# Kernel optimization log

Measured on AMD Instinct MI355X. Metric: run time of the kernel, lower is better.

## Reference

```python
import jax, jax.numpy as jnp
import numpy as np
from jax import lax

# bior3.5 decomposition low-pass filter (pywt.Wavelet('bior3.5').dec_lo)
_BIOR35_DEC_LO = [-0.013810679320049757, 0.04143203796014927, 0.052480581416189075,
                  -0.26792717880896527, -0.07181553246425873, 0.966747552403483,
                  0.966747552403483, -0.07181553246425873, -0.26792717880896527,
                  0.052480581416189075, 0.04143203796014927, -0.013810679320049757]

J = 3  # decomposition levels


def setup_inputs() -> dict:
    key = jax.random.key(0)
    x = jax.random.normal(key, (16, 64, 16384), dtype=jnp.float32)
    hac = jnp.asarray(np.array(_BIOR35_DEC_LO, dtype=np.float32))
    return {"x": x, "hac": hac}


def _afb1d(x, h0, h1):
    """Analysis filter bank: stride-2 depthwise conv over last dim.

    x: (B, C, N); h0, h1: (L,). Returns (lo, hi), each (B, C, outsize).
    Since every channel uses the same pair of filters, we fold (B, C) into
    the batch dim and run a single-input-channel, 2-output-channel conv.
    """
    B, C, N = x.shape
    L = h0.shape[0]
    outsize = (N + L - 1) // 2              # pywt 'zero' mode coeff length
    p = 2 * (outsize - 1) - N + L           # total padding needed
    if p % 2 == 1:                          # odd -> extra zero on the right
        x = jnp.pad(x, ((0, 0), (0, 0), (0, 1)))
        N += 1
        p -= 1
    half = p // 2
    xr = x.reshape(B * C, 1, N)
    k = jnp.stack([h0, h1])[:, None, :]     # (2, 1, L) -- cross-correlation, like torch
    out = lax.conv_general_dilated(xr, k, window_strides=(2,),
                                   padding=[(half, half)],
                                   dimension_numbers=('NCH', 'OIH', 'NCH'))
    lo = out[:, 0, :].reshape(B, C, outsize)
    hi = out[:, 1, :].reshape(B, C, outsize)
    return lo, hi


def reference(x, hac):
    L = hac.shape[0]
    # QMF pair: h1[i] = (-1)^(i+1) * h0[L-1-i]  (miu[::2] = -1 in torch code)
    sign = jnp.where(jnp.arange(L) % 2 == 0, -1.0, 1.0).astype(hac.dtype)
    h0 = hac
    h1 = hac[::-1] * sign
    x0 = x
    highs = []
    for _ in range(J):
        x0, x1 = _afb1d(x0, h0, h1)
        highs.append(x1)
    return (x0, *highs)
```

## Files before the change

### kernel.cpp

```cpp
#include <hip/hip_runtime.h>


#define FILT_LEN 12
#define ROWS  1024
#define N1    16384
#define O1    8197
#define O2    4104
#define O3    2057
#define NBLK  8
#define T1    1025
#define T2    513
#define T3    258
#define NTHR  256

#define XCAP    2208
#define L1CAP   1120
#define LO2_OFF 1088
#define LO2SZ   560
#define HB2_OFF 1664
#define HI3_OFF 272

typedef float vf4 __attribute__((ext_vector_type(4)));
typedef float vf2 __attribute__((ext_vector_type(2)));

constexpr int cmin(int a, int b) { return a < b ? a : b; }
constexpr int cmax(int a, int b) { return a > b ? a : b; }

__device__ __forceinline__ int sw4(int f4) { return f4 ^ ((f4 >> 3) & 7); }
__device__ __forceinline__ float4 ld4(const float* p, int f4) {
    return reinterpret_cast<const float4*>(p)[sw4(f4)];
}
__device__ __forceinline__ void st4(float* p, int f4, float4 v) {
    reinterpret_cast<float4*>(p)[sw4(f4)] = v;
}
__device__ __forceinline__ float ldss(const float* p, int j) {
    return p[(sw4(j >> 2) << 2) | (j & 3)];
}
__device__ __forceinline__ void stss(float* p, int j, float v) {
    p[(sw4(j >> 2) << 2) | (j & 3)] = v;
}
__device__ __forceinline__ void stp2(float* p, int j, float a, float b) {
    *reinterpret_cast<float2*>(p + ((sw4(j >> 2) << 2) | (j & 3))) =
        make_float2(a, b);
}

__device__ __forceinline__ void bar_lgkm() {
    asm volatile("s_waitcnt lgkmcnt(0)" ::: "memory");
    __builtin_amdgcn_s_barrier();
    asm volatile("" ::: "memory");
}

__device__ __forceinline__ void ntst(float* p, float v) {
    __builtin_nontemporal_store(v, p);
}
__device__ __forceinline__ void ntst2(float* p, float a, float b) {
    vf2 v; v.x = a; v.y = b;
    __builtin_nontemporal_store(v, reinterpret_cast<vf2*>(p));
}
__device__ __forceinline__ void ntst4(float* p, float4 u) {
    vf4 v; v.x = u.x; v.y = u.y; v.z = u.z; v.w = u.w;
    __builtin_nontemporal_store(v, reinterpret_cast<vf4*>(p));
}

template<int LO, int HI, int SOFF>
__device__ __forceinline__ void flushv(const float* s, float* g, const int tid) {
    static_assert((SOFF & 3) == 0, "stash offset f4-aligned");
    constexpr int A  = (LO + 3) & ~3;
    constexpr int Bq = HI & ~3;
    if (tid < A - LO)
        ntst(g + LO + tid, ldss(s, SOFF + LO + tid));
    if (tid >= 4 && tid < 4 + (HI - Bq))
        ntst(g + Bq + (tid - 4), ldss(s, SOFF + Bq + (tid - 4)));
    for (int i = A + 4 * tid; i < Bq; i += 4 * NTHR)
        ntst4(g + i, ld4(s, (SOFF + i) >> 2));
}

template<int HI, int SOFF>
__device__ __forceinline__ void flush2(const float* s, float* g, const int tid) {
    static_assert((SOFF & 3) == 0, "stash offset f4-aligned");
    constexpr int Bq = HI & ~1;
    for (int i = 2 * tid; i < Bq; i += 2 * NTHR) {
        const float* q = s + ((sw4((SOFF + i) >> 2) << 2) | ((SOFF + i) & 3));
        ntst2(g + i, q[0], q[1]);
    }
    if ((HI & 1) && tid == 0) ntst(g + Bq, ldss(s, SOFF + Bq));
}

__device__ __forceinline__ constexpr float h0tap(int i) {
    constexpr float H[FILT_LEN] = {
        -0.013810679320049757f, 0.04143203796014927f, 0.052480581416189075f,
        -0.26792717880896527f, -0.07181553246425873f, 0.966747552403483f,
        0.966747552403483f, -0.07181553246425873f, -0.26792717880896527f,
        0.052480581416189075f, 0.04143203796014927f, -0.013810679320049757f};
    return H[i];
}
__device__ __forceinline__ constexpr float h1tap(int i) {
    return h0tap(FILT_LEN - 1 - i) * ((i & 1) ? 1.0f : -1.0f);
}
__device__ __forceinline__ vf2 tap2(int l) {
    vf2 t; t.x = h0tap(l); t.y = h1tap(l); return t;
}

__device__ __forceinline__ void pkfma(vf2& acc, float v, int l) {
#if __has_builtin(__builtin_elementwise_fma)
    vf2 vv; vv.x = v; vv.y = v;
    acc = __builtin_elementwise_fma(vv, tap2(l), acc);
#else
    acc.x = fmaf(v, h0tap(l), acc.x);
    acc.y = fmaf(v, h1tap(l), acc.y);
#endif
}

template<int B>
struct Cfg {
    static constexpr int s1 = B * T1, e1 = cmin(s1 + T1, O1);
    static constexpr int s2 = B * T2, e2 = cmin(s2 + T2, O2);
    static constexpr int s3 = B * T3, e3 = cmin(s3 + T3, O3);
    static constexpr int c2s = cmax(0, cmin(s2, 2 * s3 - 10)) & ~3;
    static constexpr int c2e = cmin(O2, cmax(e2, 2 * e3));
    static constexpr int c1s = cmax(0, cmin(s1, 2 * c2s - 10)) & ~3;
    static constexpr int c1e = cmin(O1, cmax(e1, 2 * c2e));
    static constexpr int span1 = c1e - c1s;
    static constexpr int span2 = c2e - c2s;
    static constexpr int span3 = e3 - s3;
    static constexpr int xbase = 2 * c1s - 12;
    static constexpr int D2 = 2 * c2s - 10 - c1s + 12;
    static constexpr int ab2 = D2 & ~3, p2 = D2 & 3;
    static constexpr int D3 = 2 * s3 - 10 - c2s + 12;
    static constexpr int ab3 = D3 & ~3, p3 = D3 & 3;
    static constexpr int zt1 = L1CAP - (12 + span1);
    static constexpr int zt2 = LO2SZ - (12 + span2);
    static constexpr int o1s = s1 - c1s, o1e = e1 - c1s;
    static constexpr int o2s = s2 - c2s, o2e = e2 - c2s;

    static_assert(D2 >= 0 && D3 >= 0, "pad origin");
    static_assert((D2 & 1) == 0 && (D3 & 1) == 0, "window parity (R5 bug)");
    static_assert(p2 <= 2 && p3 <= 2, "window shift fits window array");
    static_assert((c1s & 3) == 0 && (c2s & 3) == 0, "span starts mult-of-4");
    static_assert((xbase & 3) == 0, "x staging alignment");
    static_assert(zt1 >= 0 && zt1 <= NTHR, "l1 tail zero in one pass");
    static_assert(zt2 >= 0 && zt2 <= NTHR, "lo2 tail zero in one pass");
    static_assert(span1 <= 8 * NTHR, "L1 single K=8 pass");
    static_assert(span2 <= 4 * NTHR, "L2 single K=4 pass");
    static_assert(span3 <= 2 * NTHR, "L3 single K=2 pass");
    static_assert((span2 & 3) == 0, "L2 has no tail (store path)");
    static_assert(2 * (((span1 - 1) / 8) * 8) + 28 <= XCAP, "L1 window read");
    static_assert(2 * (((span2 - 1) / 4) * 4) + ab2 + 20 <= L1CAP, "L2 window read");
    static_assert(2 * (((span3 - 1) / 2) * 2) + ab3 + 16 <= LO2SZ, "L3 window read");
    static_assert(span1 <= LO2_OFF, "hi1 stash fits");
    static_assert(HB2_OFF + span2 <= XCAP, "hi2 stash fits");
    static_assert(HI3_OFF + span3 <= L1CAP, "hi3 stash fits");
    static_assert(HI3_OFF >= span3, "lo3/hi3 disjoint");
    static_assert(o1e <= span1 && o2e <= span2, "owned range inside span");
};

template<int B>
__device__ __forceinline__ void body(
    const float* __restrict__ xrow,
    float* __restrict__ lo3r, float* __restrict__ hi1r,
    float* __restrict__ hi2r, float* __restrict__ hi3r,
    float* __restrict__ xs, float* __restrict__ l1, const int tid)
{
    using C = Cfg<B>;

    if constexpr (C::xbase >= 0 && C::xbase + XCAP <= N1) {
        st4(xs, tid,       *reinterpret_cast<const float4*>(xrow + C::xbase + 4 * tid));
        st4(xs, tid + 256, *reinterpret_cast<const float4*>(xrow + C::xbase + 1024 + 4 * tid));
        if (tid < XCAP / 4 - 512)
            st4(xs, tid + 512, *reinterpret_cast<const float4*>(xrow + C::xbase + 2048 + 4 * tid));
    } else {
        for (int i = tid; i < XCAP / 4; i += NTHR) {
            const int g0 = C::xbase + 4 * i;
            float4 v;
            if (g0 >= 0 && g0 + 4 <= N1) {
                v = *reinterpret_cast<const float4*>(xrow + g0);
            } else {
                v.x = ((unsigned)(g0 + 0) < (unsigned)N1) ? xrow[g0 + 0] : 0.f;
                v.y = ((unsigned)(g0 + 1) < (unsigned)N1) ? xrow[g0 + 1] : 0.f;
                v.z = ((unsigned)(g0 + 2) < (unsigned)N1) ? xrow[g0 + 2] : 0.f;
                v.w = ((unsigned)(g0 + 3) < (unsigned)N1) ? xrow[g0 + 3] : 0.f;
            }
            st4(xs, i, v);
        }
    }
    if (tid < 12)      stss(l1, tid, 0.f);
    if (tid < C::zt1)  stss(l1, 12 + C::span1 + tid, 0.f);
    bar_lgkm();

    float hr1[8];
    const int tt1 = tid * 8;
    if (tt1 < C::span1) {
        float w[28];
#pragma unroll
        for (int m = 0; m < 7; ++m) {
            const float4 v = ld4(xs, tid * 4 + m);
            w[4 * m + 0] = v.x; w[4 * m + 1] = v.y;
            w[4 * m + 2] = v.z; w[4 * m + 3] = v.w;
        }
        vf2 ac[8];
#pragma unroll
        for (int k = 0; k < 8; ++k) { ac[k].x = 0.f; ac[k].y = 0.f; }
#pragma unroll
        for (int l = 0; l < FILT_LEN; ++l) {
#pragma unroll
            for (int k = 0; k < 8; ++k)
                pkfma(ac[k], w[2 * k + 2 + l], l);
        }
#pragma unroll
        for (int k = 0; k < 8; ++k) hr1[k] = ac[k].y;
        if (tt1 + 8 <= C::span1) {
            st4(l1, 3 + 2 * tid, make_float4(ac[0].x, ac[1].x, ac[2].x, ac[3].x));
            st4(l1, 4 + 2 * tid, make_float4(ac[4].x, ac[5].x, ac[6].x, ac[7].x));
        } else {
#pragma unroll
            for (int k = 0; k < 8; ++k)
                if (tt1 + k < C::span1) stss(l1, 12 + tt1 + k, ac[k].x);
        }
    }
    bar_lgkm();

    if (tt1 < C::span1) {
        if (tt1 + 8 <= C::span1) {
            st4(xs, 2 * tid,     make_float4(hr1[0], hr1[1], hr1[2], hr1[3]));
            st4(xs, 2 * tid + 1, make_float4(hr1[4], hr1[5], hr1[6], hr1[7]));
        } else {
#pragma unroll
            for (int k = 0; k < 8; ++k)
                if (tt1 + k < C::span1) stss(xs, tt1 + k, hr1[k]);
        }
    }
    if (tid < 12)      stss(xs, LO2_OFF + tid, 0.f);
    if (tid < C::zt2)  stss(xs, LO2_OFF + 12 + C::span2 + tid, 0.f);

    {
        const int tt2 = tid * 4;
        if (tt2 < C::span2) {
            float w[20];
#pragma unroll
            for (int m = 0; m < 5; ++m) {
                const float4 v = ld4(l1, tid * 2 + (C::ab2 >> 2) + m);
                w[4 * m + 0] = v.x; w[4 * m + 1] = v.y;
                w[4 * m + 2] = v.z; w[4 * m + 3] = v.w;
            }
            vf2 ac[4];
#pragma unroll
            for (int k = 0; k < 4; ++k) { ac[k].x = 0.f; ac[k].y = 0.f; }
#pragma unroll
            for (int l = 0; l < FILT_LEN; ++l) {
#pragma unroll
                for (int k = 0; k < 4; ++k)
                    pkfma(ac[k], w[2 * k + l + C::p2], l);
            }
            st4(xs, 275 + tid, make_float4(ac[0].x, ac[1].x, ac[2].x, ac[3].x));
            st4(xs, 416 + tid, make_float4(ac[0].y, ac[1].y, ac[2].y, ac[3].y));
        }
    }
    bar_lgkm();

    flushv<C::o1s, C::o1e, 0>(xs, hi1r + C::c1s, tid);
    flushv<C::o2s, C::o2e, HB2_OFF>(xs, hi2r + C::c2s, tid);

    {
        const int tt3 = tid * 2;
        if (tt3 < C::span3) {
            float w[16];
#pragma unroll
            for (int m = 0; m < 4; ++m) {
                const float4 v = ld4(xs, (LO2_OFF >> 2) + tid + (C::ab3 >> 2) + m);
                w[4 * m + 0] = v.x; w[4 * m + 1] = v.y;
                w[4 * m + 2] = v.z; w[4 * m + 3] = v.w;
            }
            vf2 ac[2];
#pragma unroll
            for (int k = 0; k < 2; ++k) { ac[k].x = 0.f; ac[k].y = 0.f; }
#pragma unroll
            for (int l = 0; l < FILT_LEN; ++l) {
#pragma unroll
                for (int k = 0; k < 2; ++k)
                    pkfma(ac[k], w[2 * k + l + C::p3], l);
            }
            if (tt3 + 2 <= C::span3) {
                stp2(l1, tt3,           ac[0].x, ac[1].x);
                stp2(l1, HI3_OFF + tt3, ac[0].y, ac[1].y);
            } else {
                stss(l1, tt3, ac[0].x);
                stss(l1, HI3_OFF + tt3, ac[0].y);
            }
        }
    }
    bar_lgkm();

    flush2<C::span3, 0>(l1, lo3r + C::s3, tid);
    flush2<C::span3, HI3_OFF>(l1, hi3r + C::s3, tid);
}

__global__ __launch_bounds__(NTHR, 8) void dwt_fused_kernel(
    const float* __restrict__ x,
    float* __restrict__ lo3, float* __restrict__ hi1,
    float* __restrict__ hi2, float* __restrict__ hi3)
{
    __shared__ __align__(16) float xs[XCAP];
    __shared__ __align__(16) float l1[L1CAP];

    const int tile = blockIdx.y & 7;
    const int row  = (int)blockIdx.x * 128 + ((int)blockIdx.y >> 3);
    const int tid = threadIdx.x;
    const float* xrow = x + (size_t)row * N1;
    float* lo3r = lo3 + (size_t)row * O3;
    float* hi1r = hi1 + (size_t)row * O1;
    float* hi2r = hi2 + (size_t)row * O2;
    float* hi3r = hi3 + (size_t)row * O3;

    switch (tile) {
        case 0:  body<0>(xrow, lo3r, hi1r, hi2r, hi3r, xs, l1, tid); break;
        case 1:  body<1>(xrow, lo3r, hi1r, hi2r, hi3r, xs, l1, tid); break;
        case 2:  body<2>(xrow, lo3r, hi1r, hi2r, hi3r, xs, l1, tid); break;
        case 3:  body<3>(xrow, lo3r, hi1r, hi2r, hi3r, xs, l1, tid); break;
        case 4:  body<4>(xrow, lo3r, hi1r, hi2r, hi3r, xs, l1, tid); break;
        case 5:  body<5>(xrow, lo3r, hi1r, hi2r, hi3r, xs, l1, tid); break;
        case 6:  body<6>(xrow, lo3r, hi1r, hi2r, hi3r, xs, l1, tid); break;
        default: body<7>(xrow, lo3r, hi1r, hi2r, hi3r, xs, l1, tid); break;
    }
}

extern "C" void kernel_launch(void* const* d_in, const int* in_sizes, int n_in,
                              void* d_out, int out_size, void* d_ws, size_t ws_size,
                              hipStream_t stream)
{
    const float* x = (const float*)d_in[0];
    float* out = (float*)d_out;

    float* lo3 = out;
    float* hi1 = out + (size_t)ROWS * O3;
    float* hi2 = hi1 + (size_t)ROWS * O1;
    float* hi3 = hi2 + (size_t)ROWS * O2;

    dwt_fused_kernel<<<dim3(NBLK, ROWS), dim3(NTHR), 0, stream>>>(
        x, lo3, hi1, hi2, hi3);
}
```

Baseline: 113.8 us.

## Load level-1 windows directly from global memory, skipping LDS staging of x

Level-1 filter windows are now read straight from global memory into registers with float4 loads, so the input row is no longer staged in LDS. This drops one barrier and lets hi1 be written to xs in the same pass. The hi1 flush moves earlier so it overlaps with level-2 compute. Each thread now reads overlapping 28-float windows from global memory with a 64-byte stride, which relies on L1/L2 cache hits for the duplicated reads and may coalesce less well than the staged load.

Measured after the change: 113.4 us. No clear change (-0.3%).

```diff
diff --git a/kernel.cpp b/kernel.cpp
--- a/kernel.cpp
+++ b/kernel.cpp
@@ -132,19 +132,19 @@
     static constexpr int zt2 = LO2SZ - (12 + span2);
     static constexpr int o1s = s1 - c1s, o1e = e1 - c1s;
     static constexpr int o2s = s2 - c2s, o2e = e2 - c2s;
+    static constexpr bool interior = (xbase >= 0) && (2 * c1e <= N1);
 
     static_assert(D2 >= 0 && D3 >= 0, "pad origin");
     static_assert((D2 & 1) == 0 && (D3 & 1) == 0, "window parity (R5 bug)");
     static_assert(p2 <= 2 && p3 <= 2, "window shift fits window array");
     static_assert((c1s & 3) == 0 && (c2s & 3) == 0, "span starts mult-of-4");
-    static_assert((xbase & 3) == 0, "x staging alignment");
+    static_assert((xbase & 3) == 0, "x load alignment");
     static_assert(zt1 >= 0 && zt1 <= NTHR, "l1 tail zero in one pass");
     static_assert(zt2 >= 0 && zt2 <= NTHR, "lo2 tail zero in one pass");
     static_assert(span1 <= 8 * NTHR, "L1 single K=8 pass");
     static_assert(span2 <= 4 * NTHR, "L2 single K=4 pass");
     static_assert(span3 <= 2 * NTHR, "L3 single K=2 pass");
     static_assert((span2 & 3) == 0, "L2 has no tail (store path)");
-    static_assert(2 * (((span1 - 1) / 8) * 8) + 28 <= XCAP, "L1 window read");
     static_assert(2 * (((span2 - 1) / 4) * 4) + ab2 + 20 <= L1CAP, "L2 window read");
     static_assert(2 * (((span3 - 1) / 2) * 2) + ab3 + 16 <= LO2SZ, "L3 window read");
     static_assert(span1 <= LO2_OFF, "hi1 stash fits");
@@ -163,75 +163,68 @@
 {
     using C = Cfg<B>;
 
-    if constexpr (C::xbase >= 0 && C::xbase + XCAP <= N1) {
-        st4(xs, tid,       *reinterpret_cast<const float4*>(xrow + C::xbase + 4 * tid));
-        st4(xs, tid + 256, *reinterpret_cast<const float4*>(xrow + C::xbase + 1024 + 4 * tid));
-        if (tid < XCAP / 4 - 512)
-            st4(xs, tid + 512, *reinterpret_cast<const float4*>(xrow + C::xbase + 2048 + 4 * tid));
-    } else {
-        for (int i = tid; i < XCAP / 4; i += NTHR) {
-            const int g0 = C::xbase + 4 * i;
-            float4 v;
-            if (g0 >= 0 && g0 + 4 <= N1) {
-                v = *reinterpret_cast<const float4*>(xrow + g0);
-            } else {
-                v.x = ((unsigned)(g0 + 0) < (unsigned)N1) ? xrow[g0 + 0] : 0.f;
-                v.y = ((unsigned)(g0 + 1) < (unsigned)N1) ? xrow[g0 + 1] : 0.f;
-                v.z = ((unsigned)(g0 + 2) < (unsigned)N1) ? xrow[g0 + 2] : 0.f;
-                v.w = ((unsigned)(g0 + 3) < (unsigned)N1) ? xrow[g0 + 3] : 0.f;
-            }
-            st4(xs, i, v);
-        }
-    }
     if (tid < 12)      stss(l1, tid, 0.f);
     if (tid < C::zt1)  stss(l1, 12 + C::span1 + tid, 0.f);
-    bar_lgkm();
-
-    float hr1[8];
-    const int tt1 = tid * 8;
-    if (tt1 < C::span1) {
-        float w[28];
-#pragma unroll
-        for (int m = 0; m < 7; ++m) {
-            const float4 v = ld4(xs, tid * 4 + m);
-            w[4 * m + 0] = v.x; w[4 * m + 1] = v.y;
-            w[4 * m + 2] = v.z; w[4 * m + 3] = v.w;
-        }
-        vf2 ac[8];
-#pragma unroll
-        for (int k = 0; k < 8; ++k) { ac[k].x = 0.f; ac[k].y = 0.f; }
-#pragma unroll
-        for (int l = 0; l < FILT_LEN; ++l) {
-#pragma unroll
-            for (int k = 0; k < 8; ++k)
-                pkfma(ac[k], w[2 * k + 2 + l], l);
-        }
-#pragma unroll
-        for (int k = 0; k < 8; ++k) hr1[k] = ac[k].y;
-        if (tt1 + 8 <= C::span1) {
-            st4(l1, 3 + 2 * tid, make_float4(ac[0].x, ac[1].x, ac[2].x, ac[3].x));
-            st4(l1, 4 + 2 * tid, make_float4(ac[4].x, ac[5].x, ac[6].x, ac[7].x));
-        } else {
-#pragma unroll
-            for (int k = 0; k < 8; ++k)
-                if (tt1 + k < C::span1) stss(l1, 12 + tt1 + k, ac[k].x);
-        }
-    }
-    bar_lgkm();
-
-    if (tt1 < C::span1) {
-        if (tt1 + 8 <= C::span1) {
-            st4(xs, 2 * tid,     make_float4(hr1[0], hr1[1], hr1[2], hr1[3]));
-            st4(xs, 2 * tid + 1, make_float4(hr1[4], hr1[5], hr1[6], hr1[7]));
-        } else {
-#pragma unroll
-            for (int k = 0; k < 8; ++k)
-                if (tt1 + k < C::span1) stss(xs, tt1 + k, hr1[k]);
-        }
-    }
     if (tid < 12)      stss(xs, LO2_OFF + tid, 0.f);
     if (tid < C::zt2)  stss(xs, LO2_OFF + 12 + C::span2 + tid, 0.f);
 
+    {
+        const int tt1 = tid * 8;
+        if (tt1 < C::span1) {
+            float w[28];
+            if constexpr (C::interior) {
+                const float* wp = xrow + C::xbase + 16 * tid;
+#pragma unroll
+                for (int m = 0; m < 7; ++m) {
+                    const float4 v = *reinterpret_cast<const float4*>(wp + 4 * m);
+                    w[4 * m + 0] = v.x; w[4 * m + 1] = v.y;
+                    w[4 * m + 2] = v.z; w[4 * m + 3] = v.w;
+                }
+            } else {
+#pragma unroll
+                for (int m = 0; m < 7; ++m) {
+                    const int g0 = C::xbase + 16 * tid + 4 * m;
+                    float4 v;
+                    if (g0 >= 0 && g0 + 4 <= N1) {
+                        v = *reinterpret_cast<const float4*>(xrow + g0);
+                    } else {
+                        v.x = ((unsigned)(g0 + 0) < (unsigned)N1) ? xrow[g0 + 0] : 0.f;
+                        v.y = ((unsigned)(g0 + 1) < (unsigned)N1) ? xrow[g0 + 1] : 0.f;
+                        v.z = ((unsigned)(g0 + 2) < (unsigned)N1) ? xrow[g0 + 2] : 0.f;
+                        v.w = ((unsigned)(g0 + 3) < (unsigned)N1) ? xrow[g0 + 3] : 0.f;
+                    }
+                    w[4 * m + 0] = v.x; w[4 * m + 1] = v.y;
+                    w[4 * m + 2] = v.z; w[4 * m + 3] = v.w;
+                }
+            }
+            vf2 ac[8];
+#pragma unroll
+            for (int k = 0; k < 8; ++k) { ac[k].x = 0.f; ac[k].y = 0.f; }
+#pragma unroll
+            for (int l = 0; l < FILT_LEN; ++l) {
+#pragma unroll
+                for (int k = 0; k < 8; ++k)
+                    pkfma(ac[k], w[2 * k + 2 + l], l);
+            }
+            if (tt1 + 8 <= C::span1) {
+                st4(l1, 3 + 2 * tid, make_float4(ac[0].x, ac[1].x, ac[2].x, ac[3].x));
+                st4(l1, 4 + 2 * tid, make_float4(ac[4].x, ac[5].x, ac[6].x, ac[7].x));
+                st4(xs, 2 * tid,     make_float4(ac[0].y, ac[1].y, ac[2].y, ac[3].y));
+                st4(xs, 2 * tid + 1, make_float4(ac[4].y, ac[5].y, ac[6].y, ac[7].y));
+            } else {
+#pragma unroll
+                for (int k = 0; k < 8; ++k) {
+                    if (tt1 + k < C::span1) {
+                        stss(l1, 12 + tt1 + k, ac[k].x);
+                        stss(xs, tt1 + k, ac[k].y);
+                    }
+                }
+            }
+        }
+    }
+    bar_lgkm();
+
+    flushv<C::o1s, C::o1e, 0>(xs, hi1r + C::c1s, tid);
     {
         const int tt2 = tid * 4;
         if (tt2 < C::span2) {
@@ -257,9 +250,7 @@
     }
     bar_lgkm();
 
-    flushv<C::o1s, C::o1e, 0>(xs, hi1r + C::c1s, tid);
     flushv<C::o2s, C::o2e, HB2_OFF>(xs, hi2r + C::c2s, tid);
-
     {
         const int tt3 = tid * 2;
         if (tt3 < C::span3) {
```
